# Optimization experiments

Hardware: AMD Instinct MI355X
Metric: run time of the kernel (lower is better)

## Reference

```python
import jax, jax.numpy as jnp
import numpy as np

N_NODES = 20000
N_EDGES = 160000
IN_F = 128
HID_HEADS, HID_CH = 32, 32
OUT_EMB = 64
NEG_SLOPE = 0.2


def setup_inputs() -> dict:
    key = jax.random.key(0)
    ks = jax.random.split(key, 8)
    x = jax.random.normal(ks[0], (N_NODES, IN_F), dtype=jnp.float32)
    edge_index = jax.random.randint(ks[1], (2, N_EDGES), 0, N_NODES, dtype=jnp.int32)
    W1 = jax.random.normal(ks[2], (IN_F, HID_HEADS * HID_CH), dtype=jnp.float32) / np.sqrt(IN_F)
    att_src1 = jax.random.normal(ks[3], (HID_HEADS, HID_CH), dtype=jnp.float32) / np.sqrt(HID_CH)
    att_dst1 = jax.random.normal(ks[4], (HID_HEADS, HID_CH), dtype=jnp.float32) / np.sqrt(HID_CH)
    b1 = jnp.zeros((HID_HEADS * HID_CH,), dtype=jnp.float32)
    W2 = jax.random.normal(ks[5], (HID_HEADS * HID_CH, OUT_EMB), dtype=jnp.float32) / np.sqrt(HID_HEADS * HID_CH)
    att_src2 = jax.random.normal(ks[6], (1, OUT_EMB), dtype=jnp.float32) / np.sqrt(OUT_EMB)
    att_dst2 = jax.random.normal(ks[7], (1, OUT_EMB), dtype=jnp.float32) / np.sqrt(OUT_EMB)
    b2 = jnp.zeros((OUT_EMB,), dtype=jnp.float32)
    return {"x": x, "edge_index": edge_index, "W1": W1, "att_src1": att_src1,
            "att_dst1": att_dst1, "b1": b1, "W2": W2, "att_src2": att_src2,
            "att_dst2": att_dst2, "b2": b2}


def _gat_conv(x, src, dst, W, a_src, a_dst, b, n_nodes):
    # PyG GATConv (eval mode): per-head linear, edge attention, segment softmax over
    # incoming edges of each target node, weighted scatter-sum, concat heads + bias.
    H, C = a_src.shape
    h = (x @ W).reshape(-1, H, C)                       # [N, H, C]
    e_s = jnp.einsum('nhc,hc->nh', h, a_src)            # [N, H]
    e_d = jnp.einsum('nhc,hc->nh', h, a_dst)            # [N, H]
    e = jax.nn.leaky_relu(e_s[src] + e_d[dst], NEG_SLOPE)  # [E, H]
    m = jax.ops.segment_max(e, dst, num_segments=n_nodes)  # [N, H]
    m = jnp.where(jnp.isfinite(m), m, jnp.zeros_like(m))   # nodes w/o in-edges
    ex = jnp.exp(e - m[dst])                            # [E, H]
    s = jax.ops.segment_sum(ex, dst, num_segments=n_nodes)
    alpha = ex / (s[dst] + 1e-16)                       # [E, H]
    msg = h[src] * alpha[:, :, None]                    # [E, H, C]
    out = jax.ops.segment_sum(msg, dst, num_segments=n_nodes)  # [N, H, C]
    return out.reshape(n_nodes, H * C) + b


def reference(x, edge_index, W1, att_src1, att_dst1, b1, W2, att_src2, att_dst2, b2):
    n = x.shape[0]
    loops = jnp.arange(n, dtype=edge_index.dtype)
    src = jnp.concatenate([edge_index[0], loops])  # PyG adds self-loops by default
    dst = jnp.concatenate([edge_index[1], loops])
    h = jax.nn.elu(_gat_conv(x, src, dst, W1, att_src1, att_dst1, b1, n))
    out = _gat_conv(h, src, dst, W2, att_src2, att_dst2, b2, n)
    return out
```

## Files before the change

### kernel.cpp

```cpp
#include <hip/hip_runtime.h>
#include <hip/hip_bf16.h>
#include <math.h>

typedef __attribute__((ext_vector_type(8))) short bf16x8;
typedef __attribute__((ext_vector_type(4))) float f32x4;
typedef __attribute__((ext_vector_type(8))) unsigned short u16x8;

__device__ inline float bf2f(unsigned short u) {
    union { float f; unsigned int i; } c; c.i = ((unsigned int)u) << 16; return c.f;
}
__device__ inline unsigned short f2bf(float f) {
    union { float f; unsigned int i; } c; c.f = f;
    unsigned int r = c.i + 0x7fffu + ((c.i >> 16) & 1u);
    return (unsigned short)(r >> 16);
}

__global__ void prep_count(const float* __restrict__ x, unsigned short* __restrict__ xb,
                           const float* __restrict__ W1, unsigned short* __restrict__ W1T,
                           const float* __restrict__ W2, unsigned short* __restrict__ W2T,
                           const int* __restrict__ ei, int* __restrict__ counts,
                           int count4, int E0, int n) {
    int idx = blockIdx.x * blockDim.x + threadIdx.x;
    const int n1 = 128 * 1024;
    const int n2 = 1024 * 64;
    if (idx < count4) {
        float4 v = *(const float4*)&x[(size_t)idx * 4];
        ushort4 o;
        o.x = f2bf(v.x); o.y = f2bf(v.y); o.z = f2bf(v.z); o.w = f2bf(v.w);
        *(ushort4*)&xb[(size_t)idx * 4] = o;
    } else if (idx < count4 + n1) {
        int i1 = idx - count4;
        int nn = i1 / 128, kk = i1 - nn * 128;
        W1T[i1] = f2bf(W1[(size_t)kk * 1024 + nn]);
    } else if (idx < count4 + n1 + n2) {
        int i2 = idx - count4 - n1;
        int nn = i2 / 1024, kk = i2 - nn * 1024;
        W2T[i2] = f2bf(W2[(size_t)kk * 64 + nn]);
    } else {
        int e = idx - count4 - n1 - n2;
        int Etot = E0 + n;
        if (e < Etot) {
            int dst = (e < E0) ? ei[E0 + e] : (e - E0);
            atomicAdd(&counts[dst], 1);
        }
    }
}

__global__ void scan_excl(const int* __restrict__ counts, int* __restrict__ offsets, int n) {
    __shared__ int wpre[16];
    __shared__ int total_s;
    __shared__ int running_s;
    int tid = threadIdx.x, lane = tid & 63, w = tid >> 6;
    if (tid == 0) running_s = 0;
    __syncthreads();
    for (int base = 0; base < n; base += 1024) {
        int i = base + tid;
        int v = (i < n) ? counts[i] : 0;
        int incl = v;
        #pragma unroll
        for (int d = 1; d < 64; d <<= 1) {
            int t = __shfl_up(incl, d);
            if (lane >= d) incl += t;
        }
        if (lane == 63) wpre[w] = incl;
        __syncthreads();
        if (w == 0) {
            int s = (lane < 16) ? wpre[lane] : 0;
            int sc = s;
            #pragma unroll
            for (int d = 1; d < 16; d <<= 1) {
                int t = __shfl_up(sc, d);
                if (lane >= d) sc += t;
            }
            if (lane < 16) wpre[lane] = sc - s;
            if (lane == 15) total_s = sc;
        }
        __syncthreads();
        int r = running_s;
        if (i < n) offsets[i] = r + wpre[w] + incl - v;
        __syncthreads();
        if (tid == 0) running_s = r + total_s;
        __syncthreads();
    }
    if (tid == 0) offsets[n] = running_s;
}

__global__ __launch_bounds__(256) void fill_gemm1(const int* __restrict__ ei,
                                                  const int* __restrict__ offsets,
                                                  int* __restrict__ cursor,
                                                  int* __restrict__ srcs,
                                                  int E0, int n,
                                                  const unsigned short* __restrict__ A,
                                                  const unsigned short* __restrict__ BT,
                                                  unsigned short* __restrict__ C,
                                                  const float* __restrict__ asrc,
                                                  const float* __restrict__ adst,
                                                  float* __restrict__ es,
                                                  float* __restrict__ ed,
                                                  int M, int FB) {
    int tid = threadIdx.x;
    if ((int)blockIdx.x < FB) {
        int e = blockIdx.x * 256 + tid;
        int Etot = E0 + n;
        if (e >= Etot) return;
        int src, dst;
        if (e < E0) { src = ei[e]; dst = ei[E0 + e]; }
        else        { src = dst = e - E0; }
        int pos = offsets[dst] + atomicAdd(&cursor[dst], 1);
        srcs[pos] = src;
        return;
    }
    const int K = 128, N = 1024;
    int gb = blockIdx.x - FB;
    int bx = gb >> 4, by = gb & 15;
    int wid = tid >> 6, lane = tid & 63;
    int wm = wid >> 1, wn = wid & 1;
    int m0b = bx * 64, n0b = by * 64;
    int m0 = m0b + wm * 32;
    int n0 = n0b + wn * 32;
    int lr = lane & 15;
    int q  = lane >> 4;
    int lk = q * 8;

    int ra0 = min(m0 + lr, M - 1);
    int ra1 = min(m0 + 16 + lr, M - 1);
    const unsigned short* pa[2] = { A + (size_t)ra0 * K + lk, A + (size_t)ra1 * K + lk };
    const unsigned short* pb[2] = { BT + (size_t)(n0 + lr) * K + lk,
                                    BT + (size_t)(n0 + 16 + lr) * K + lk };

    bf16x8 av[2][4], bv[2][4];
    #pragma unroll
    for (int i = 0; i < 2; ++i)
        #pragma unroll
        for (int s = 0; s < 4; ++s) {
            av[i][s] = *(const bf16x8*)(pa[i] + s * 32);
            bv[i][s] = *(const bf16x8*)(pb[i] + s * 32);
        }
    f32x4 acc00 = {0,0,0,0}, acc01 = {0,0,0,0}, acc10 = {0,0,0,0}, acc11 = {0,0,0,0};
    #pragma unroll
    for (int s = 0; s < 4; ++s) {
        acc00 = __builtin_amdgcn_mfma_f32_16x16x32_bf16(av[0][s], bv[0][s], acc00, 0, 0, 0);
        acc01 = __builtin_amdgcn_mfma_f32_16x16x32_bf16(av[0][s], bv[1][s], acc01, 0, 0, 0);
        acc10 = __builtin_amdgcn_mfma_f32_16x16x32_bf16(av[1][s], bv[0][s], acc10, 0, 0, 0);
        acc11 = __builtin_amdgcn_mfma_f32_16x16x32_bf16(av[1][s], bv[1][s], acc11, 0, 0, 0);
    }
    __shared__ unsigned short ct[64][68];
    int srow = q * 4;
    #pragma unroll
    for (int r = 0; r < 4; ++r) {
        ct[wm * 32 + srow + r][wn * 32 + lr]           = f2bf(acc00[r]);
        ct[wm * 32 + srow + r][wn * 32 + 16 + lr]      = f2bf(acc01[r]);
        ct[wm * 32 + 16 + srow + r][wn * 32 + lr]      = f2bf(acc10[r]);
        ct[wm * 32 + 16 + srow + r][wn * 32 + 16 + lr] = f2bf(acc11[r]);
    }
    __syncthreads();
    {
        int row = tid >> 2, cs = (tid & 3) * 16;
        int gr = m0b + row;
        if (gr < M) {
            u16x8 v0, v1;
            #pragma unroll
            for (int j = 0; j < 8; ++j) { v0[j] = ct[row][cs + j]; v1[j] = ct[row][cs + 8 + j]; }
            *(u16x8*)&C[(size_t)gr * N + n0b + cs]     = v0;
            *(u16x8*)&C[(size_t)gr * N + n0b + cs + 8] = v1;
        }
    }
    int head = by * 2 + wn;
    float as_lo = asrc[head * 32 + lr], as_hi = asrc[head * 32 + 16 + lr];
    float ad_lo = adst[head * 32 + lr], ad_hi = adst[head * 32 + 16 + lr];
    #pragma unroll
    for (int X = 0; X < 2; ++X) {
        f32x4 ac0 = X ? acc10 : acc00;
        f32x4 ac1 = X ? acc11 : acc01;
        #pragma unroll
        for (int r = 0; r < 4; ++r) {
            float ps = ac0[r] * as_lo + ac1[r] * as_hi;
            float pd = ac0[r] * ad_lo + ac1[r] * ad_hi;
            #pragma unroll
            for (int msk = 1; msk < 16; msk <<= 1) {
                ps += __shfl_xor(ps, msk);
                pd += __shfl_xor(pd, msk);
            }
            int row = m0 + X * 16 + q * 4 + r;
            if (lr == 0 && row < M) {
                es[row * 32 + head] = ps;
                ed[row * 32 + head] = pd;
            }
        }
    }
}

__global__ __launch_bounds__(256) void gemm2_fused(const unsigned short* __restrict__ A,
                                                   const unsigned short* __restrict__ BT,
                                                   unsigned short* __restrict__ C,
                                                   const float* __restrict__ asrc,
                                                   const float* __restrict__ adst,
                                                   float* __restrict__ es,
                                                   float* __restrict__ ed, int M) {
    const int K = 1024;
    int tid = threadIdx.x, wid = tid >> 6, lane = tid & 63;
    int m0 = blockIdx.x * 32;
    int lr = lane & 15, q = lane >> 4, lk = q * 8;
    int k0 = wid * 256;

    const unsigned short* pa0 = A + (size_t)(m0 + lr) * K + k0 + lk;
    const unsigned short* pa1 = A + (size_t)(m0 + 16 + lr) * K + k0 + lk;
    const unsigned short* pb0 = BT + (size_t)(0  + lr) * K + k0 + lk;
    const unsigned short* pb1 = BT + (size_t)(16 + lr) * K + k0 + lk;
    const unsigned short* pb2 = BT + (size_t)(32 + lr) * K + k0 + lk;
    const unsigned short* pb3 = BT + (size_t)(48 + lr) * K + k0 + lk;

    f32x4 acc[2][4] = {};
    for (int k = 0; k < 256; k += 64) {
        bf16x8 a0  = *(const bf16x8*)(pa0 + k);
        bf16x8 a1  = *(const bf16x8*)(pa1 + k);
        bf16x8 a0b = *(const bf16x8*)(pa0 + k + 32);
        bf16x8 a1b = *(const bf16x8*)(pa1 + k + 32);
        bf16x8 b0  = *(const bf16x8*)(pb0 + k);
        bf16x8 b0b = *(const bf16x8*)(pb0 + k + 32);
        acc[0][0] = __builtin_amdgcn_mfma_f32_16x16x32_bf16(a0,  b0,  acc[0][0], 0, 0, 0);
        acc[1][0] = __builtin_amdgcn_mfma_f32_16x16x32_bf16(a1,  b0,  acc[1][0], 0, 0, 0);
        acc[0][0] = __builtin_amdgcn_mfma_f32_16x16x32_bf16(a0b, b0b, acc[0][0], 0, 0, 0);
        acc[1][0] = __builtin_amdgcn_mfma_f32_16x16x32_bf16(a1b, b0b, acc[1][0], 0, 0, 0);
        bf16x8 b1  = *(const bf16x8*)(pb1 + k);
        bf16x8 b1b = *(const bf16x8*)(pb1 + k + 32);
        acc[0][1] = __builtin_amdgcn_mfma_f32_16x16x32_bf16(a0,  b1,  acc[0][1], 0, 0, 0);
        acc[1][1] = __builtin_amdgcn_mfma_f32_16x16x32_bf16(a1,  b1,  acc[1][1], 0, 0, 0);
        acc[0][1] = __builtin_amdgcn_mfma_f32_16x16x32_bf16(a0b, b1b, acc[0][1], 0, 0, 0);
        acc[1][1] = __builtin_amdgcn_mfma_f32_16x16x32_bf16(a1b, b1b, acc[1][1], 0, 0, 0);
        bf16x8 b2  = *(const bf16x8*)(pb2 + k);
        bf16x8 b2b = *(const bf16x8*)(pb2 + k + 32);
        acc[0][2] = __builtin_amdgcn_mfma_f32_16x16x32_bf16(a0,  b2,  acc[0][2], 0, 0, 0);
        acc[1][2] = __builtin_amdgcn_mfma_f32_16x16x32_bf16(a1,  b2,  acc[1][2], 0, 0, 0);
        acc[0][2] = __builtin_amdgcn_mfma_f32_16x16x32_bf16(a0b, b2b, acc[0][2], 0, 0, 0);
        acc[1][2] = __builtin_amdgcn_mfma_f32_16x16x32_bf16(a1b, b2b, acc[1][2], 0, 0, 0);
        bf16x8 b3  = *(const bf16x8*)(pb3 + k);
        bf16x8 b3b = *(const bf16x8*)(pb3 + k + 32);
        acc[0][3] = __builtin_amdgcn_mfma_f32_16x16x32_bf16(a0,  b3,  acc[0][3], 0, 0, 0);
        acc[1][3] = __builtin_amdgcn_mfma_f32_16x16x32_bf16(a1,  b3,  acc[1][3], 0, 0, 0);
        acc[0][3] = __builtin_amdgcn_mfma_f32_16x16x32_bf16(a0b, b3b, acc[0][3], 0, 0, 0);
        acc[1][3] = __builtin_amdgcn_mfma_f32_16x16x32_bf16(a1b, b3b, acc[1][3], 0, 0, 0);
    }
    __shared__ float red[4][32][64];
    #pragma unroll
    for (int rf = 0; rf < 2; ++rf)
        #pragma unroll
        for (int cf = 0; cf < 4; ++cf)
            #pragma unroll
            for (int i = 0; i < 4; ++i)
                red[wid][rf * 16 + q * 4 + i][cf * 16 + lr] = acc[rf][cf][i];
    __syncthreads();
    int r = tid >> 3, c0 = (tid & 7) * 8;
    float v[8];
    #pragma unroll
    for (int j = 0; j < 8; ++j)
        v[j] = red[0][r][c0 + j] + red[1][r][c0 + j] + red[2][r][c0 + j] + red[3][r][c0 + j];
    u16x8 o8;
    float ps = 0.f, pd = 0.f;
    #pragma unroll
    for (int j = 0; j < 8; ++j) {
        o8[j] = f2bf(v[j]);
        ps += v[j] * asrc[c0 + j];
        pd += v[j] * adst[c0 + j];
    }
    int row = m0 + r;
    *(u16x8*)&C[(size_t)row * 64 + c0] = o8;
    #pragma unroll
    for (int msk = 1; msk < 8; msk <<= 1) {
        ps += __shfl_xor(ps, msk);
        pd += __shfl_xor(pd, msk);
    }
    if ((tid & 7) == 0) { es[row] = ps; ed[row] = pd; }
}

__global__ __launch_bounds__(256) void gat1_agg(const unsigned short* __restrict__ hb,
                                                const float* __restrict__ es,
                                                const float* __restrict__ ed,
                                                const int* __restrict__ offsets,
                                                const int* __restrict__ srcs,
                                                const float* __restrict__ b1,
                                                unsigned short* __restrict__ out, int n) {
    int node = blockIdx.x;
    int tid = threadIdx.x;
    int h2 = tid & 31, j2 = tid >> 5;
    int ep = tid >> 7, t2 = tid & 127;
    int head = t2 >> 2, c8 = (t2 & 3) * 8;
    int hoff = head * 32 + c8;

    __shared__ unsigned short lds_et[128][32];
    __shared__ float sed[32];
    __shared__ float red[4][32];
    __shared__ float sinv_s[32];
    __shared__ float lcomb[128][9];

    int beg = offsets[node], end = offsets[node + 1];
    if (tid < 32) sed[tid] = ed[node * 32 + tid];
    __syncthreads();
    float edh = sed[h2];
    float ssum = 0.f;
    float a[8] = {0.f,0.f,0.f,0.f,0.f,0.f,0.f,0.f};

    for (int c0 = beg; c0 < end; c0 += 128) {
        int lim = min(128, end - c0);
        for (int eloc = j2; eloc < lim; eloc += 8) {
            int s = srcs[c0 + eloc];
            float ev = es[s * 32 + h2] + edh;
            ev = ev > 0.f ? ev : 0.2f * ev;
            unsigned short w16 = f2bf(__expf(ev));
            lds_et[eloc][h2] = w16;
            ssum += bf2f(w16);
        }
        __syncthreads();
        int eloc = ep;
        for (; eloc + 2 < lim; eloc += 4) {
            int s0 = srcs[c0 + eloc], s1 = srcs[c0 + eloc + 2];
            float t0 = bf2f(lds_et[eloc][head]);
            float t1 = bf2f(lds_et[eloc + 2][head]);
            u16x8 h0 = *(const u16x8*)&hb[(size_t)s0 * 1024 + hoff];
            u16x8 h1 = *(const u16x8*)&hb[(size_t)s1 * 1024 + hoff];
            #pragma unroll
            for (int j = 0; j < 8; ++j) a[j] += t0 * bf2f(h0[j]) + t1 * bf2f(h1[j]);
        }
        if (eloc < lim) {
            int s0 = srcs[c0 + eloc];
            float t0 = bf2f(lds_et[eloc][head]);
            u16x8 h0 = *(const u16x8*)&hb[(size_t)s0 * 1024 + hoff];
            #pragma unroll
            for (int j = 0; j < 8; ++j) a[j] += t0 * bf2f(h0[j]);
        }
        __syncthreads();
    }

    ssum += __shfl_xor(ssum, 32);
    int w = tid >> 6;
    if ((tid & 63) < 32) red[w][h2] = ssum;
    if (ep == 1) {
        #pragma unroll
        for (int j = 0; j < 8; ++j) lcomb[t2][j] = a[j];
    }
    __syncthreads();
    if (tid < 32) {
        float s = red[0][tid] + red[1][tid] + red[2][tid] + red[3][tid];
        sinv_s[tid] = 1.0f / (s + 1e-16f);
    }
    __syncthreads();
    if (ep == 0) {
        float si = sinv_s[head];
        float4 bl = *(const float4*)&b1[hoff];
        float4 bh = *(const float4*)&b1[hoff + 4];
        float bb[8] = {bl.x, bl.y, bl.z, bl.w, bh.x, bh.y, bh.z, bh.w};
        u16x8 o8;
        #pragma unroll
        for (int j = 0; j < 8; ++j) {
            float r = (a[j] + lcomb[t2][j]) * si + bb[j];
            r = r > 0.f ? r : expm1f(r);
            o8[j] = f2bf(r);
        }
        *(u16x8*)&out[(size_t)node * 1024 + hoff] = o8;
    }
}

__global__ __launch_bounds__(256) void gat2_agg(const unsigned short* __restrict__ hb2,
                                                const float* __restrict__ es,
                                                const float* __restrict__ ed,
                                                const int* __restrict__ offsets,
                                                const int* __restrict__ srcs,
                                                const float* __restrict__ b2,
                                                float* __restrict__ out, int n) {
    int w = threadIdx.x >> 6;
    int node = blockIdx.x * 4 + w;
    int lane = threadIdx.x & 63;
    __shared__ float lt[4][64];
    if (node >= n) return;
    int beg = offsets[node], end = offsets[node + 1];
    float edv = ed[node];
    float ssum = 0.f, acc = 0.f;
    for (int c0 = beg; c0 < end; c0 += 64) {
        int lim = min(64, end - c0);
        float t = 0.f;
        if (lane < lim) {
            int s = srcs[c0 + lane];
            float ev = es[s] + edv;
            ev = ev > 0.f ? ev : 0.2f * ev;
            t = __expf(ev);
        }
        lt[w][lane] = t;
        ssum += t;
        asm volatile("s_waitcnt lgkmcnt(0)" ::: "memory");
        int jj = 0;
        for (; jj + 3 < lim; jj += 4) {
            int s0 = srcs[c0 + jj], s1 = srcs[c0 + jj + 1];
            int s2 = srcs[c0 + jj + 2], s3 = srcs[c0 + jj + 3];
            acc += lt[w][jj]     * bf2f(hb2[(size_t)s0 * 64 + lane])
                 + lt[w][jj + 1] * bf2f(hb2[(size_t)s1 * 64 + lane])
                 + lt[w][jj + 2] * bf2f(hb2[(size_t)s2 * 64 + lane])
                 + lt[w][jj + 3] * bf2f(hb2[(size_t)s3 * 64 + lane]);
        }
        for (; jj < lim; ++jj) {
            acc += lt[w][jj] * bf2f(hb2[(size_t)srcs[c0 + jj] * 64 + lane]);
        }
    }
    #pragma unroll
    for (int o = 1; o < 64; o <<= 1) ssum += __shfl_xor(ssum, o);
    out[(size_t)node * 64 + lane] = acc * (1.0f / (ssum + 1e-16f)) + b2[lane];
}

extern "C" void kernel_launch(void* const* d_in, const int* in_sizes, int n_in,
                              void* d_out, int out_size, void* d_ws, size_t ws_size,
                              hipStream_t stream) {
    const float* x        = (const float*)d_in[0];
    const int*   ei       = (const int*)d_in[1];
    const float* W1       = (const float*)d_in[2];
    const float* att_src1 = (const float*)d_in[3];
    const float* att_dst1 = (const float*)d_in[4];
    const float* b1       = (const float*)d_in[5];
    const float* W2       = (const float*)d_in[6];
    const float* att_src2 = (const float*)d_in[7];
    const float* att_dst2 = (const float*)d_in[8];
    const float* b2       = (const float*)d_in[9];
    float* out = (float*)d_out;

    int n  = in_sizes[0] / 128;
    int E0 = in_sizes[1] / 2;
    int Etot = E0 + n;

    float* ws = (float*)d_ws;
    size_t off = 0;
    unsigned short* hb1 = (unsigned short*)(ws + off); off += (size_t)n * 512;
    unsigned short* hact = (unsigned short*)(ws + off); off += (size_t)n * 512;
    unsigned short* hb2 = (unsigned short*)(ws + off); off += (size_t)n * 32;
    unsigned short* xb  = (unsigned short*)(ws + off); off += (size_t)n * 64;
    unsigned short* W1T = (unsigned short*)(ws + off); off += 1024 * 128 / 2;
    unsigned short* W2T = (unsigned short*)(ws + off); off += 64 * 1024 / 2;
    float* es1  = ws + off; off += (size_t)n * 32;
    float* ed1  = ws + off; off += (size_t)n * 32;
    int* counts  = (int*)(ws + off); off += n;
    int* cursor  = (int*)(ws + off); off += n;
    int* offsets = (int*)(ws + off); off += n + 8;
    int* srcs    = (int*)(ws + off); off += Etot;
    float* es2 = es1;
    float* ed2 = ed1;

    int count4 = n * 128 / 4;
    int prep_total = count4 + 128 * 1024 + 64 * 1024 + Etot;
    int FB = (Etot + 255) / 256;
    int GB = ((n + 63) / 64) * 16;

    hipMemsetAsync(counts, 0, 2 * (size_t)n * sizeof(int), stream);
    prep_count<<<(prep_total + 255) / 256, 256, 0, stream>>>(
        x, xb, W1, W1T, W2, W2T, ei, counts, count4, E0, n);
    scan_excl<<<1, 1024, 0, stream>>>(counts, offsets, n);
    fill_gemm1<<<FB + GB, 256, 0, stream>>>(ei, offsets, cursor, srcs, E0, n,
                                            xb, W1T, hb1, att_src1, att_dst1,
                                            es1, ed1, n, FB);
    gat1_agg<<<n, 256, 0, stream>>>(hb1, es1, ed1, offsets, srcs, b1, hact, n);
    gemm2_fused<<<n / 32, 256, 0, stream>>>(hact, W2T, hb2, att_src2, att_dst2, es2, ed2, n);
    gat2_agg<<<(n + 3) / 4, 256, 0, stream>>>(hb2, es2, ed2, offsets, srcs, b2, out, n);
}
```

Measured before the change: 192.4 us.

## Store layer-1 features head-major and aggregate per head for gather locality

GEMM1 now writes projected features and attention logits in head-major layout ([head][node][32] and [head][node]). A new aggregation kernel assigns each block one head and 32 target nodes, with 8 threads per node accumulating 4 channels each without shared memory or barriers. The goal is that the random neighbour gathers for one head touch a compact, cache-resident slice instead of striding through 2KB rows. In exchange, the CSR edge list and offsets are read once per head, and each thread walks its edges serially.

```diff
diff --git a/kernel.cpp b/kernel.cpp
--- a/kernel.cpp
+++ b/kernel.cpp
@@ -92,11 +92,11 @@
                                                   int E0, int n,
                                                   const unsigned short* __restrict__ A,
                                                   const unsigned short* __restrict__ BT,
-                                                  unsigned short* __restrict__ C,
+                                                  unsigned short* __restrict__ Ct,
                                                   const float* __restrict__ asrc,
                                                   const float* __restrict__ adst,
-                                                  float* __restrict__ es,
-                                                  float* __restrict__ ed,
+                                                  float* __restrict__ es_t,
+                                                  float* __restrict__ ed_t,
                                                   int M, int FB) {
     int tid = threadIdx.x;
     if ((int)blockIdx.x < FB) {
@@ -110,14 +110,14 @@
         srcs[pos] = src;
         return;
     }
-    const int K = 128, N = 1024;
+    const int K = 128;
     int gb = blockIdx.x - FB;
     int bx = gb >> 4, by = gb & 15;
     int wid = tid >> 6, lane = tid & 63;
     int wm = wid >> 1, wn = wid & 1;
-    int m0b = bx * 64, n0b = by * 64;
+    int m0b = bx * 64;
     int m0 = m0b + wm * 32;
-    int n0 = n0b + wn * 32;
+    int n0 = by * 64 + wn * 32;
     int lr = lane & 15;
     int q  = lane >> 4;
     int lk = q * 8;
@@ -155,14 +155,19 @@
     }
     __syncthreads();
     {
-        int row = tid >> 2, cs = (tid & 3) * 16;
-        int gr = m0b + row;
+        int hg = tid >> 7, t2 = tid & 127;
+        int r = t2 >> 1, chh = (t2 & 1) * 16;
+        int gr = m0b + r;
         if (gr < M) {
             u16x8 v0, v1;
             #pragma unroll
-            for (int j = 0; j < 8; ++j) { v0[j] = ct[row][cs + j]; v1[j] = ct[row][cs + 8 + j]; }
-            *(u16x8*)&C[(size_t)gr * N + n0b + cs]     = v0;
-            *(u16x8*)&C[(size_t)gr * N + n0b + cs + 8] = v1;
+            for (int j = 0; j < 8; ++j) {
+                v0[j] = ct[r][hg * 32 + chh + j];
+                v1[j] = ct[r][hg * 32 + chh + 8 + j];
+            }
+            size_t base = (size_t)(by * 2 + hg) * M * 32 + (size_t)gr * 32 + chh;
+            *(u16x8*)&Ct[base]     = v0;
+            *(u16x8*)&Ct[base + 8] = v1;
         }
     }
     int head = by * 2 + wn;
@@ -183,11 +188,72 @@
             }
             int row = m0 + X * 16 + q * 4 + r;
             if (lr == 0 && row < M) {
-                es[row * 32 + head] = ps;
-                ed[row * 32 + head] = pd;
+                es_t[(size_t)head * M + row] = ps;
+                ed_t[(size_t)head * M + row] = pd;
             }
         }
     }
+}
+
+__global__ __launch_bounds__(256) void gat1_agg_t(const unsigned short* __restrict__ hb_t,
+                                                  const float* __restrict__ es_t,
+                                                  const float* __restrict__ ed_t,
+                                                  const int* __restrict__ offsets,
+                                                  const int* __restrict__ srcs,
+                                                  const float* __restrict__ b1,
+                                                  unsigned short* __restrict__ out,
+                                                  int n) {
+    int bid = blockIdx.x;
+    int hh = bid & 31, chunk = bid >> 5;
+    int tid = threadIdx.x;
+    int ni = tid >> 3, j = tid & 7, ch4 = j * 4;
+    int node = chunk * 32 + ni;
+    if (node >= n) return;
+    const unsigned short* hs = hb_t + (size_t)hh * n * 32;
+    const float* ess = es_t + (size_t)hh * n;
+    float edv = ed_t[(size_t)hh * n + node];
+    int beg = offsets[node], end = offsets[node + 1];
+    float a0 = 0.f, a1 = 0.f, a2 = 0.f, a3 = 0.f, ssum = 0.f;
+    int e = beg;
+    for (; e + 1 < end; e += 2) {
+        int s0 = srcs[e], s1 = srcs[e + 1];
+        float ev0 = ess[s0] + edv;
+        float ev1 = ess[s1] + edv;
+        ev0 = ev0 > 0.f ? ev0 : 0.2f * ev0;
+        ev1 = ev1 > 0.f ? ev1 : 0.2f * ev1;
+        float t0 = __expf(ev0), t1 = __expf(ev1);
+        ssum += t0 + t1;
+        ushort4 h0 = *(const ushort4*)&hs[(size_t)s0 * 32 + ch4];
+        ushort4 h1 = *(const ushort4*)&hs[(size_t)s1 * 32 + ch4];
+        a0 += t0 * bf2f(h0.x) + t1 * bf2f(h1.x);
+        a1 += t0 * bf2f(h0.y) + t1 * bf2f(h1.y);
+        a2 += t0 * bf2f(h0.z) + t1 * bf2f(h1.z);
+        a3 += t0 * bf2f(h0.w) + t1 * bf2f(h1.w);
+    }
+    if (e < end) {
+        int s0 = srcs[e];
+        float ev0 = ess[s0] + edv;
+        ev0 = ev0 > 0.f ? ev0 : 0.2f * ev0;
+        float t0 = __expf(ev0);
+        ssum += t0;
+        ushort4 h0 = *(const ushort4*)&hs[(size_t)s0 * 32 + ch4];
+        a0 += t0 * bf2f(h0.x); a1 += t0 * bf2f(h0.y);
+        a2 += t0 * bf2f(h0.z); a3 += t0 * bf2f(h0.w);
+    }
+    float si = 1.0f / (ssum + 1e-16f);
+    int o = hh * 32 + ch4;
+    float4 bb = *(const float4*)&b1[o];
+    float r0 = a0 * si + bb.x;
+    float r1 = a1 * si + bb.y;
+    float r2 = a2 * si + bb.z;
+    float r3 = a3 * si + bb.w;
+    r0 = r0 > 0.f ? r0 : expm1f(r0);
+    r1 = r1 > 0.f ? r1 : expm1f(r1);
+    r2 = r2 > 0.f ? r2 : expm1f(r2);
+    r3 = r3 > 0.f ? r3 : expm1f(r3);
+    ushort4 o4;
+    o4.x = f2bf(r0); o4.y = f2bf(r1); o4.z = f2bf(r2); o4.w = f2bf(r3);
+    *(ushort4*)&out[(size_t)node * 1024 + o] = o4;
 }
 
 __global__ __launch_bounds__(256) void gemm2_fused(const unsigned short* __restrict__ A,
@@ -273,93 +339,6 @@
     if ((tid & 7) == 0) { es[row] = ps; ed[row] = pd; }
 }
 
-__global__ __launch_bounds__(256) void gat1_agg(const unsigned short* __restrict__ hb,
-                                                const float* __restrict__ es,
-                                                const float* __restrict__ ed,
-                                                const int* __restrict__ offsets,
-                                                const int* __restrict__ srcs,
-                                                const float* __restrict__ b1,
-                                                unsigned short* __restrict__ out, int n) {
-    int node = blockIdx.x;
-    int tid = threadIdx.x;
-    int h2 = tid & 31, j2 = tid >> 5;
-    int ep = tid >> 7, t2 = tid & 127;
-    int head = t2 >> 2, c8 = (t2 & 3) * 8;
-    int hoff = head * 32 + c8;
-
-    __shared__ unsigned short lds_et[128][32];
-    __shared__ float sed[32];
-    __shared__ float red[4][32];
-    __shared__ float sinv_s[32];
-    __shared__ float lcomb[128][9];
-
-    int beg = offsets[node], end = offsets[node + 1];
-    if (tid < 32) sed[tid] = ed[node * 32 + tid];
-    __syncthreads();
-    float edh = sed[h2];
-    float ssum = 0.f;
-    float a[8] = {0.f,0.f,0.f,0.f,0.f,0.f,0.f,0.f};
-
-    for (int c0 = beg; c0 < end; c0 += 128) {
-        int lim = min(128, end - c0);
-        for (int eloc = j2; eloc < lim; eloc += 8) {
-            int s = srcs[c0 + eloc];
-            float ev = es[s * 32 + h2] + edh;
-            ev = ev > 0.f ? ev : 0.2f * ev;
-            unsigned short w16 = f2bf(__expf(ev));
-            lds_et[eloc][h2] = w16;
-            ssum += bf2f(w16);
-        }
-        __syncthreads();
-        int eloc = ep;
-        for (; eloc + 2 < lim; eloc += 4) {
-            int s0 = srcs[c0 + eloc], s1 = srcs[c0 + eloc + 2];
-            float t0 = bf2f(lds_et[eloc][head]);
-            float t1 = bf2f(lds_et[eloc + 2][head]);
-            u16x8 h0 = *(const u16x8*)&hb[(size_t)s0 * 1024 + hoff];
-            u16x8 h1 = *(const u16x8*)&hb[(size_t)s1 * 1024 + hoff];
-            #pragma unroll
-            for (int j = 0; j < 8; ++j) a[j] += t0 * bf2f(h0[j]) + t1 * bf2f(h1[j]);
-        }
-        if (eloc < lim) {
-            int s0 = srcs[c0 + eloc];
-            float t0 = bf2f(lds_et[eloc][head]);
-            u16x8 h0 = *(const u16x8*)&hb[(size_t)s0 * 1024 + hoff];
-            #pragma unroll
-            for (int j = 0; j < 8; ++j) a[j] += t0 * bf2f(h0[j]);
-        }
-        __syncthreads();
-    }
-
-    ssum += __shfl_xor(ssum, 32);
-    int w = tid >> 6;
-    if ((tid & 63) < 32) red[w][h2] = ssum;
-    if (ep == 1) {
-        #pragma unroll
-        for (int j = 0; j < 8; ++j) lcomb[t2][j] = a[j];
-    }
-    __syncthreads();
-    if (tid < 32) {
-        float s = red[0][tid] + red[1][tid] + red[2][tid] + red[3][tid];
-        sinv_s[tid] = 1.0f / (s + 1e-16f);
-    }
-    __syncthreads();
-    if (ep == 0) {
-        float si = sinv_s[head];
-        float4 bl = *(const float4*)&b1[hoff];
-        float4 bh = *(const float4*)&b1[hoff + 4];
-        float bb[8] = {bl.x, bl.y, bl.z, bl.w, bh.x, bh.y, bh.z, bh.w};
-        u16x8 o8;
-        #pragma unroll
-        for (int j = 0; j < 8; ++j) {
-            float r = (a[j] + lcomb[t2][j]) * si + bb[j];
-            r = r > 0.f ? r : expm1f(r);
-            o8[j] = f2bf(r);
-        }
-        *(u16x8*)&out[(size_t)node * 1024 + hoff] = o8;
-    }
-}
-
 __global__ __launch_bounds__(256) void gat2_agg(const unsigned short* __restrict__ hb2,
                                                 const float* __restrict__ es,
                                                 const float* __restrict__ ed,
@@ -426,20 +405,20 @@
 
     float* ws = (float*)d_ws;
     size_t off = 0;
-    unsigned short* hb1 = (unsigned short*)(ws + off); off += (size_t)n * 512;
+    unsigned short* hb1t = (unsigned short*)(ws + off); off += (size_t)n * 512;
     unsigned short* hact = (unsigned short*)(ws + off); off += (size_t)n * 512;
     unsigned short* hb2 = (unsigned short*)(ws + off); off += (size_t)n * 32;
     unsigned short* xb  = (unsigned short*)(ws + off); off += (size_t)n * 64;
     unsigned short* W1T = (unsigned short*)(ws + off); off += 1024 * 128 / 2;
     unsigned short* W2T = (unsigned short*)(ws + off); off += 64 * 1024 / 2;
-    float* es1  = ws + off; off += (size_t)n * 32;
-    float* ed1  = ws + off; off += (size_t)n * 32;
+    float* es1t = ws + off; off += (size_t)n * 32;
+    float* ed1t = ws + off; off += (size_t)n * 32;
     int* counts  = (int*)(ws + off); off += n;
     int* cursor  = (int*)(ws + off); off += n;
     int* offsets = (int*)(ws + off); off += n + 8;
     int* srcs    = (int*)(ws + off); off += Etot;
-    float* es2 = es1;
-    float* ed2 = ed1;
+    float* es2 = es1t;
+    float* ed2 = ed1t;
 
     int count4 = n * 128 / 4;
     int prep_total = count4 + 128 * 1024 + 64 * 1024 + Etot;
@@ -451,9 +430,10 @@
         x, xb, W1, W1T, W2, W2T, ei, counts, count4, E0, n);
     scan_excl<<<1, 1024, 0, stream>>>(counts, offsets, n);
     fill_gemm1<<<FB + GB, 256, 0, stream>>>(ei, offsets, cursor, srcs, E0, n,
-                                            xb, W1T, hb1, att_src1, att_dst1,
-                                            es1, ed1, n, FB);
-    gat1_agg<<<n, 256, 0, stream>>>(hb1, es1, ed1, offsets, srcs, b1, hact, n);
+                                            xb, W1T, hb1t, att_src1, att_dst1,
+                                            es1t, ed1t, n, FB);
+    gat1_agg_t<<<((n + 31) / 32) * 32, 256, 0, stream>>>(
+        hb1t, es1t, ed1t, offsets, srcs, b1, hact, n);
     gemm2_fused<<<n / 32, 256, 0, stream>>>(hact, W2T, hb2, att_src2, att_dst2, es2, ed2, n);
     gat2_agg<<<(n + 3) / 4, 256, 0, stream>>>(hb2, es2, ed2, offsets, srcs, b2, out, n);
 }
```

Result: slower. 212.7 us (+10.6%).
